# Optimization experiments

Hardware: AMD Instinct MI355X
Metric: run time of the kernel (lower is better)

## Reference

```python
import jax, jax.numpy as jnp
import numpy as np

Q_DIM, K_DIM, H_DIM = 24, 24, 64


def setup_inputs() -> dict:
    key = jax.random.key(0)
    ks = jax.random.split(key, 11)
    B, N, D_OUT = 2048, 512, 128
    s = lambda fan_in: 1.0 / np.sqrt(fan_in)
    inp = {
        "future_weather_patch": jax.random.normal(ks[0], (B, Q_DIM), jnp.float32),
        "past_weather_patches": jax.random.normal(ks[1], (B, N, K_DIM), jnp.float32),
        "transformer_output": jax.random.normal(ks[2], (B, N, D_OUT), jnp.float32),
        # W_Q: Linear(q,h) -> Tanh -> Linear(h,h)
        "wq1": jax.random.uniform(ks[3], (Q_DIM, H_DIM), jnp.float32, -s(Q_DIM), s(Q_DIM)),
        "bq1": jax.random.uniform(ks[4], (H_DIM,), jnp.float32, -s(Q_DIM), s(Q_DIM)),
        "wq2": jax.random.uniform(ks[5], (H_DIM, H_DIM), jnp.float32, -s(H_DIM), s(H_DIM)),
        "bq2": jax.random.uniform(ks[6], (H_DIM,), jnp.float32, -s(H_DIM), s(H_DIM)),
        # W_K: Linear(k,h) -> Tanh -> Linear(h,h)
        "wk1": jax.random.uniform(ks[7], (K_DIM, H_DIM), jnp.float32, -s(K_DIM), s(K_DIM)),
        "bk1": jax.random.uniform(ks[8], (H_DIM,), jnp.float32, -s(K_DIM), s(K_DIM)),
        "wk2": jax.random.uniform(ks[9], (H_DIM, H_DIM), jnp.float32, -s(H_DIM), s(H_DIM)),
        "bk2": jax.random.uniform(ks[10], (H_DIM,), jnp.float32, -s(H_DIM), s(H_DIM)),
    }
    return inp


def reference(future_weather_patch, past_weather_patches, transformer_output,
              wq1, bq1, wq2, bq2, wk1, bk1, wk2, bk2):
    scale = 1.0 / np.sqrt(H_DIM).astype(np.float32)
    # Q: [B, H]  (Linear-Tanh-Linear on the single future patch)
    q = jnp.tanh(future_weather_patch @ wq1 + bq1) @ wq2 + bq2
    # K: [B, N, H]
    k = jnp.tanh(past_weather_patches @ wk1 + bk1) @ wk2 + bk2
    # score: [B, 1, N] = Q . K^T * scale
    score = jnp.einsum("bh,bnh->bn", q, k) * scale
    attn_weights = jax.nn.softmax(score, axis=-1)[:, None, :]  # [B, 1, N]
    # context: [B, D] = attn @ transformer_output
    context = jnp.einsum("bn,bnd->bd", attn_weights[:, 0, :], transformer_output)
    return context, attn_weights
```

## Files before the change

### kernel.cpp

```cpp
#include <hip/hip_runtime.h>
#include <math.h>

#define QD 24
#define KD 24
#define HD 64
#define NN 512
#define DO 128
#define CHUNK 128
#define NCHUNK (NN / CHUNK)

__device__ __forceinline__ float fast_tanh(float x) {
    float ax = __builtin_fabsf(x);
    float t  = __builtin_amdgcn_exp2f(-2.885390081777927f * ax);
    float r  = (1.0f - t) * __builtin_amdgcn_rcpf(1.0f + t);
    return __builtin_copysignf(r, x);
}

__global__ __launch_bounds__(256, 8) void fused_attn(
    const float* __restrict__ fwp,
    const float* __restrict__ pwp,
    const float* __restrict__ to,
    const float* __restrict__ wq1, const float* __restrict__ bq1,
    const float* __restrict__ wq2, const float* __restrict__ bq2,
    const float* __restrict__ wk1, const float* __restrict__ bk1,
    const float* __restrict__ wk2,
    float* __restrict__ out_ctx,
    float* __restrict__ out_attn)
{
    const int b = blockIdx.x;
    const int t = threadIdx.x;

    __shared__ float p_all[NN];
    __shared__ float xf[QD];
    __shared__ float h1[HD];
    __shared__ float qv[HD];
    __shared__ float qks[HD];
    __shared__ float4 part[4][32];

    if (t < QD) xf[t] = fwp[(size_t)b * QD + t];
    __syncthreads();
    if (t < HD) {
        float a = bq1[t];
#pragma unroll
        for (int k = 0; k < QD; ++k) a = fmaf(xf[k], wq1[k * HD + t], a);
        h1[t] = fast_tanh(a);
    }
    __syncthreads();
    if (t < HD) {
        float a = bq2[t];
#pragma unroll
        for (int i = 0; i < HD; ++i) a = fmaf(h1[i], wq2[i * HD + t], a);
        qv[t] = a;
    }
    __syncthreads();
    if (t < HD) {
        float s = 0.0f;
#pragma unroll
        for (int h = 0; h < HD; ++h) s = fmaf(wk2[t * HD + h], qv[h], s);
        qks[t] = s * 0.18033688011112042f;
    }
    __syncthreads();

    float Mb = 0.0f;
#pragma unroll
    for (int h = 0; h < HD; ++h) Mb += __builtin_fabsf(qks[h]);

    const bool is_prod = (t < 128);
    const int ct = t - 128;
    const int g  = ct & 31;
    const int r  = (ct >> 5) & 3;

    const float4* trow = reinterpret_cast<const float4*>(to + (size_t)b * NN * DO) + g;
    float4 acc = make_float4(0.f, 0.f, 0.f, 0.f);

    auto consume = [&](int cc) {
        const int n0 = cc * CHUNK + r * 32;
#pragma unroll 8
        for (int i = 0; i < 32; ++i) {
            const int n = n0 + i;
            const float p = p_all[n];
            float4 v = trow[(size_t)n * (DO / 4)];
            acc.x = fmaf(p, v.x, acc.x);
            acc.y = fmaf(p, v.y, acc.y);
            acc.z = fmaf(p, v.z, acc.z);
            acc.w = fmaf(p, v.w, acc.w);
        }
    };

    const float4* wk1_4 = reinterpret_cast<const float4*>(wk1);
    const float4* bk1_4 = reinterpret_cast<const float4*>(bk1);
    const float4* qks_4 = reinterpret_cast<const float4*>(qks);

    for (int c = 0; c < NCHUNK; ++c) {
        if (is_prod) {
            const int n = c * CHUNK + t;
            const float* prow = pwp + ((size_t)b * NN + n) * KD;
            float x[KD];
#pragma unroll
            for (int i = 0; i < KD / 4; ++i) {
                float4 v = reinterpret_cast<const float4*>(prow)[i];
                x[4 * i + 0] = v.x; x[4 * i + 1] = v.y;
                x[4 * i + 2] = v.z; x[4 * i + 3] = v.w;
            }
            float sc = 0.0f;
#pragma unroll 2
            for (int j4 = 0; j4 < HD / 4; ++j4) {
                float4 bb = bk1_4[j4];
                float a0 = bb.x, a1 = bb.y, a2 = bb.z, a3 = bb.w;
#pragma unroll
                for (int k = 0; k < KD; ++k) {
                    float4 w = wk1_4[k * (HD / 4) + j4];
                    a0 = fmaf(x[k], w.x, a0); a1 = fmaf(x[k], w.y, a1);
                    a2 = fmaf(x[k], w.z, a2); a3 = fmaf(x[k], w.w, a3);
                }
                float4 qq = qks_4[j4];
                sc = fmaf(fast_tanh(a0), qq.x, sc);
                sc = fmaf(fast_tanh(a1), qq.y, sc);
                sc = fmaf(fast_tanh(a2), qq.z, sc);
                sc = fmaf(fast_tanh(a3), qq.w, sc);
            }
            p_all[n] = __builtin_amdgcn_exp2f(sc - Mb);
        } else if (c > 0) {
            consume(c - 1);
        }
        __syncthreads();
    }

    float invL = 0.0f;
    if (!is_prod) {
        consume(NCHUNK - 1);
        part[r][g] = acc;
    } else if (t < 64) {
        float l = 0.0f;
#pragma unroll
        for (int i = 0; i < NN / 64; ++i) l += p_all[t + 64 * i];
#pragma unroll
        for (int o = 32; o > 0; o >>= 1) l += __shfl_xor(l, o, 64);
        invL = __builtin_amdgcn_rcpf(l);
        float* oa = out_attn + (size_t)b * NN;
#pragma unroll
        for (int i = 0; i < NN / 64; ++i) oa[t + 64 * i] = p_all[t + 64 * i] * invL;
    }
    __syncthreads();

    if (t < 32) {
        float4 r0 = part[0][t], r1 = part[1][t], r2 = part[2][t], r3 = part[3][t];
        float4 o;
        o.x = ((r0.x + r1.x) + (r2.x + r3.x)) * invL;
        o.y = ((r0.y + r1.y) + (r2.y + r3.y)) * invL;
        o.z = ((r0.z + r1.z) + (r2.z + r3.z)) * invL;
        o.w = ((r0.w + r1.w) + (r2.w + r3.w)) * invL;
        reinterpret_cast<float4*>(out_ctx + (size_t)b * DO)[t] = o;
    }
}

extern "C" void kernel_launch(void* const* d_in, const int* in_sizes, int n_in,
                              void* d_out, int out_size, void* d_ws, size_t ws_size,
                              hipStream_t stream) {
    const float* fwp = (const float*)d_in[0];
    const float* pwp = (const float*)d_in[1];
    const float* to  = (const float*)d_in[2];
    const float* wq1 = (const float*)d_in[3];
    const float* bq1 = (const float*)d_in[4];
    const float* wq2 = (const float*)d_in[5];
    const float* bq2 = (const float*)d_in[6];
    const float* wk1 = (const float*)d_in[7];
    const float* bk1 = (const float*)d_in[8];
    const float* wk2 = (const float*)d_in[9];

    float* out = (float*)d_out;
    const int B = in_sizes[0] / QD;

    fused_attn<<<B, 256, 0, stream>>>(fwp, pwp, to, wq1, bq1, wq2, bq2,
                                      wk1, bk1, wk2,
                                      out, out + (size_t)B * DO);
}
```

Baseline: 138.6 us.

## Use 512-thread blocks with one key row per thread, drop producer/consumer split

```diff
diff --git a/kernel.cpp b/kernel.cpp
--- a/kernel.cpp
+++ b/kernel.cpp
@@ -6,8 +6,7 @@
 #define HD 64
 #define NN 512
 #define DO 128
-#define CHUNK 128
-#define NCHUNK (NN / CHUNK)
+#define BT 512
 
 __device__ __forceinline__ float fast_tanh(float x) {
     float ax = __builtin_fabsf(x);
@@ -16,7 +15,7 @@
     return __builtin_copysignf(r, x);
 }
 
-__global__ __launch_bounds__(256, 8) void fused_attn(
+__global__ __launch_bounds__(BT, 4) void fused_attn(
     const float* __restrict__ fwp,
     const float* __restrict__ pwp,
     const float* __restrict__ to,
@@ -30,12 +29,21 @@
     const int b = blockIdx.x;
     const int t = threadIdx.x;
 
-    __shared__ float p_all[NN];
     __shared__ float xf[QD];
     __shared__ float h1[HD];
     __shared__ float qv[HD];
     __shared__ float qks[HD];
-    __shared__ float4 part[4][32];
+    __shared__ float p_all[NN];
+    __shared__ float s_red[8];
+    __shared__ float4 part[16][32];
+
+    const float* prow = pwp + ((size_t)b * NN + t) * KD;
+    float4 xv0 = reinterpret_cast<const float4*>(prow)[0];
+    float4 xv1 = reinterpret_cast<const float4*>(prow)[1];
+    float4 xv2 = reinterpret_cast<const float4*>(prow)[2];
+    float4 xv3 = reinterpret_cast<const float4*>(prow)[3];
+    float4 xv4 = reinterpret_cast<const float4*>(prow)[4];
+    float4 xv5 = reinterpret_cast<const float4*>(prow)[5];
 
     if (t < QD) xf[t] = fwp[(size_t)b * QD + t];
     __syncthreads();
@@ -65,91 +73,74 @@
 #pragma unroll
     for (int h = 0; h < HD; ++h) Mb += __builtin_fabsf(qks[h]);
 
-    const bool is_prod = (t < 128);
-    const int ct = t - 128;
-    const int g  = ct & 31;
-    const int r  = (ct >> 5) & 3;
-
-    const float4* trow = reinterpret_cast<const float4*>(to + (size_t)b * NN * DO) + g;
-    float4 acc = make_float4(0.f, 0.f, 0.f, 0.f);
-
-    auto consume = [&](int cc) {
-        const int n0 = cc * CHUNK + r * 32;
-#pragma unroll 8
-        for (int i = 0; i < 32; ++i) {
-            const int n = n0 + i;
-            const float p = p_all[n];
-            float4 v = trow[(size_t)n * (DO / 4)];
-            acc.x = fmaf(p, v.x, acc.x);
-            acc.y = fmaf(p, v.y, acc.y);
-            acc.z = fmaf(p, v.z, acc.z);
-            acc.w = fmaf(p, v.w, acc.w);
-        }
-    };
+    float x[KD];
+    x[0]=xv0.x; x[1]=xv0.y; x[2]=xv0.z; x[3]=xv0.w;
+    x[4]=xv1.x; x[5]=xv1.y; x[6]=xv1.z; x[7]=xv1.w;
+    x[8]=xv2.x; x[9]=xv2.y; x[10]=xv2.z; x[11]=xv2.w;
+    x[12]=xv3.x; x[13]=xv3.y; x[14]=xv3.z; x[15]=xv3.w;
+    x[16]=xv4.x; x[17]=xv4.y; x[18]=xv4.z; x[19]=xv4.w;
+    x[20]=xv5.x; x[21]=xv5.y; x[22]=xv5.z; x[23]=xv5.w;
 
     const float4* wk1_4 = reinterpret_cast<const float4*>(wk1);
     const float4* bk1_4 = reinterpret_cast<const float4*>(bk1);
     const float4* qks_4 = reinterpret_cast<const float4*>(qks);
 
-    for (int c = 0; c < NCHUNK; ++c) {
-        if (is_prod) {
-            const int n = c * CHUNK + t;
-            const float* prow = pwp + ((size_t)b * NN + n) * KD;
-            float x[KD];
+    float sc = 0.0f;
+#pragma unroll 2
+    for (int j4 = 0; j4 < HD / 4; ++j4) {
+        float4 bb = bk1_4[j4];
+        float a0 = bb.x, a1 = bb.y, a2 = bb.z, a3 = bb.w;
 #pragma unroll
-            for (int i = 0; i < KD / 4; ++i) {
-                float4 v = reinterpret_cast<const float4*>(prow)[i];
-                x[4 * i + 0] = v.x; x[4 * i + 1] = v.y;
-                x[4 * i + 2] = v.z; x[4 * i + 3] = v.w;
-            }
-            float sc = 0.0f;
-#pragma unroll 2
-            for (int j4 = 0; j4 < HD / 4; ++j4) {
-                float4 bb = bk1_4[j4];
-                float a0 = bb.x, a1 = bb.y, a2 = bb.z, a3 = bb.w;
+        for (int k = 0; k < KD; ++k) {
+            float4 w = wk1_4[k * (HD / 4) + j4];
+            a0 = fmaf(x[k], w.x, a0); a1 = fmaf(x[k], w.y, a1);
+            a2 = fmaf(x[k], w.z, a2); a3 = fmaf(x[k], w.w, a3);
+        }
+        float4 qq = qks_4[j4];
+        sc = fmaf(fast_tanh(a0), qq.x, sc);
+        sc = fmaf(fast_tanh(a1), qq.y, sc);
+        sc = fmaf(fast_tanh(a2), qq.z, sc);
+        sc = fmaf(fast_tanh(a3), qq.w, sc);
+    }
+    const float p = __builtin_amdgcn_exp2f(sc - Mb);
+    p_all[t] = p;
+
+    float l = p;
 #pragma unroll
-                for (int k = 0; k < KD; ++k) {
-                    float4 w = wk1_4[k * (HD / 4) + j4];
-                    a0 = fmaf(x[k], w.x, a0); a1 = fmaf(x[k], w.y, a1);
-                    a2 = fmaf(x[k], w.z, a2); a3 = fmaf(x[k], w.w, a3);
-                }
-                float4 qq = qks_4[j4];
-                sc = fmaf(fast_tanh(a0), qq.x, sc);
-                sc = fmaf(fast_tanh(a1), qq.y, sc);
-                sc = fmaf(fast_tanh(a2), qq.z, sc);
-                sc = fmaf(fast_tanh(a3), qq.w, sc);
-            }
-            p_all[n] = __builtin_amdgcn_exp2f(sc - Mb);
-        } else if (c > 0) {
-            consume(c - 1);
-        }
-        __syncthreads();
+    for (int o = 32; o > 0; o >>= 1) l += __shfl_xor(l, o, 64);
+    if ((t & 63) == 0) s_red[t >> 6] = l;
+    __syncthreads();
+    const float L = ((s_red[0] + s_red[1]) + (s_red[2] + s_red[3]))
+                  + ((s_red[4] + s_red[5]) + (s_red[6] + s_red[7]));
+    const float invL = __builtin_amdgcn_rcpf(L);
+    out_attn[(size_t)b * NN + t] = p * invL;
+
+    const int g  = t & 31;
+    const int np = t >> 5;
+    const float4* trow = reinterpret_cast<const float4*>(to + (size_t)b * NN * DO) + g;
+    float4 acc = make_float4(0.f, 0.f, 0.f, 0.f);
+#pragma unroll 8
+    for (int i = 0; i < 32; ++i) {
+        const int n = np * 32 + i;
+        const float pp = p_all[n];
+        float4 v = trow[(size_t)n * (DO / 4)];
+        acc.x = fmaf(pp, v.x, acc.x);
+        acc.y = fmaf(pp, v.y, acc.y);
+        acc.z = fmaf(pp, v.z, acc.z);
+        acc.w = fmaf(pp, v.w, acc.w);
     }
-
-    float invL = 0.0f;
-    if (!is_prod) {
-        consume(NCHUNK - 1);
-        part[r][g] = acc;
-    } else if (t < 64) {
-        float l = 0.0f;
-#pragma unroll
-        for (int i = 0; i < NN / 64; ++i) l += p_all[t + 64 * i];
-#pragma unroll
-        for (int o = 32; o > 0; o >>= 1) l += __shfl_xor(l, o, 64);
-        invL = __builtin_amdgcn_rcpf(l);
-        float* oa = out_attn + (size_t)b * NN;
-#pragma unroll
-        for (int i = 0; i < NN / 64; ++i) oa[t + 64 * i] = p_all[t + 64 * i] * invL;
-    }
+    part[np][g] = acc;
     __syncthreads();
 
     if (t < 32) {
-        float4 r0 = part[0][t], r1 = part[1][t], r2 = part[2][t], r3 = part[3][t];
+        float4 r = part[0][t];
+#pragma unroll
+        for (int q = 1; q < 16; ++q) {
+            float4 v = part[q][t];
+            r.x += v.x; r.y += v.y; r.z += v.z; r.w += v.w;
+        }
         float4 o;
-        o.x = ((r0.x + r1.x) + (r2.x + r3.x)) * invL;
-        o.y = ((r0.y + r1.y) + (r2.y + r3.y)) * invL;
-        o.z = ((r0.z + r1.z) + (r2.z + r3.z)) * invL;
-        o.w = ((r0.w + r1.w) + (r2.w + r3.w)) * invL;
+        o.x = r.x * invL; o.y = r.y * invL; o.z = r.z * invL; o.w = r.w * invL;
         reinterpret_cast<float4*>(out_ctx + (size_t)b * DO)[t] = o;
     }
 }
@@ -171,7 +162,7 @@
     float* out = (float*)d_out;
     const int B = in_sizes[0] / QD;
 
-    fused_attn<<<B, 256, 0, stream>>>(fwp, pwp, to, wq1, bq1, wq2, bq2,
-                                      wk1, bk1, wk2,
-                                      out, out + (size_t)B * DO);
+    fused_attn<<<B, BT, 0, stream>>>(fwp, pwp, to, wq1, bq1, wq2, bq2,
+                                     wk1, bk1, wk2,
+                                     out, out + (size_t)B * DO);
 }
```

Result: slower. 153.6 us (+10.8%).

## Split query projection into a separate kernel and lower occupancy hint

Applied to the files above, without the earlier changes.

```diff
diff --git a/kernel.cpp b/kernel.cpp
--- a/kernel.cpp
+++ b/kernel.cpp
@@ -16,54 +16,61 @@
     return __builtin_copysignf(r, x);
 }
 
-__global__ __launch_bounds__(256, 8) void fused_attn(
+__global__ __launch_bounds__(64) void qk_proj(
     const float* __restrict__ fwp,
+    const float* __restrict__ wq1, const float* __restrict__ bq1,
+    const float* __restrict__ wq2, const float* __restrict__ bq2,
+    const float* __restrict__ wk2,
+    float* __restrict__ qks_g, float* __restrict__ Mb_g)
+{
+    const int b = blockIdx.x;
+    const int j = threadIdx.x;
+    __shared__ float xf[QD];
+    __shared__ float h1[HD];
+    __shared__ float qv[HD];
+    if (j < QD) xf[j] = fwp[(size_t)b * QD + j];
+    __syncthreads();
+    float acc = bq1[j];
+#pragma unroll
+    for (int k = 0; k < QD; ++k) acc = fmaf(xf[k], wq1[k * HD + j], acc);
+    h1[j] = fast_tanh(acc);
+    __syncthreads();
+    acc = bq2[j];
+#pragma unroll
+    for (int i = 0; i < HD; ++i) acc = fmaf(h1[i], wq2[i * HD + j], acc);
+    qv[j] = acc;
+    __syncthreads();
+    float s = 0.0f;
+#pragma unroll
+    for (int h = 0; h < HD; ++h) s = fmaf(wk2[j * HD + h], qv[h], s);
+    const float val = s * 0.18033688011112042f;
+    qks_g[(size_t)b * HD + j] = val;
+    float mb = __builtin_fabsf(val);
+#pragma unroll
+    for (int o = 32; o > 0; o >>= 1) mb += __shfl_xor(mb, o, 64);
+    if (j == 0) Mb_g[b] = mb;
+}
+
+__global__ __launch_bounds__(256, 4) void prodcons_attn(
     const float* __restrict__ pwp,
     const float* __restrict__ to,
-    const float* __restrict__ wq1, const float* __restrict__ bq1,
-    const float* __restrict__ wq2, const float* __restrict__ bq2,
-    const float* __restrict__ wk1, const float* __restrict__ bk1,
-    const float* __restrict__ wk2,
+    const float* __restrict__ wk1,
+    const float* __restrict__ bk1,
+    const float* __restrict__ qks_g,
+    const float* __restrict__ Mb_g,
     float* __restrict__ out_ctx,
     float* __restrict__ out_attn)
 {
     const int b = blockIdx.x;
     const int t = threadIdx.x;
 
-    __shared__ float p_all[NN];
-    __shared__ float xf[QD];
-    __shared__ float h1[HD];
-    __shared__ float qv[HD];
-    __shared__ float qks[HD];
+    __shared__ float  p_all[NN];
+    __shared__ float  qks[HD];
     __shared__ float4 part[4][32];
 
-    if (t < QD) xf[t] = fwp[(size_t)b * QD + t];
+    if (t < HD) qks[t] = qks_g[(size_t)b * HD + t];
+    const float Mb = Mb_g[b];
     __syncthreads();
-    if (t < HD) {
-        float a = bq1[t];
-#pragma unroll
-        for (int k = 0; k < QD; ++k) a = fmaf(xf[k], wq1[k * HD + t], a);
-        h1[t] = fast_tanh(a);
-    }
-    __syncthreads();
-    if (t < HD) {
-        float a = bq2[t];
-#pragma unroll
-        for (int i = 0; i < HD; ++i) a = fmaf(h1[i], wq2[i * HD + t], a);
-        qv[t] = a;
-    }
-    __syncthreads();
-    if (t < HD) {
-        float s = 0.0f;
-#pragma unroll
-        for (int h = 0; h < HD; ++h) s = fmaf(wk2[t * HD + h], qv[h], s);
-        qks[t] = s * 0.18033688011112042f;
-    }
-    __syncthreads();
-
-    float Mb = 0.0f;
-#pragma unroll
-    for (int h = 0; h < HD; ++h) Mb += __builtin_fabsf(qks[h]);
 
     const bool is_prod = (t < 128);
     const int ct = t - 128;
@@ -97,11 +104,9 @@
             const float* prow = pwp + ((size_t)b * NN + n) * KD;
             float x[KD];
 #pragma unroll
-            for (int i = 0; i < KD / 4; ++i) {
-                float4 v = reinterpret_cast<const float4*>(prow)[i];
-                x[4 * i + 0] = v.x; x[4 * i + 1] = v.y;
-                x[4 * i + 2] = v.z; x[4 * i + 3] = v.w;
-            }
+            for (int i = 0; i < KD / 4; ++i)
+                reinterpret_cast<float4*>(x)[i] =
+                    reinterpret_cast<const float4*>(prow)[i];
             float sc = 0.0f;
 #pragma unroll 2
             for (int j4 = 0; j4 < HD / 4; ++j4) {
@@ -168,10 +173,15 @@
     const float* bk1 = (const float*)d_in[8];
     const float* wk2 = (const float*)d_in[9];
 
-    float* out = (float*)d_out;
-    const int B = in_sizes[0] / QD;
+    float* out      = (float*)d_out;
+    const int B     = in_sizes[0] / QD;
+    float* out_ctx  = out;
+    float* out_attn = out + (size_t)B * DO;
 
-    fused_attn<<<B, 256, 0, stream>>>(fwp, pwp, to, wq1, bq1, wq2, bq2,
-                                      wk1, bk1, wk2,
-                                      out, out + (size_t)B * DO);
+    float* qks_g = (float*)d_ws;
+    float* Mb_g  = qks_g + (size_t)B * HD;
+
+    qk_proj<<<B, 64, 0, stream>>>(fwp, wq1, bq1, wq2, bq2, wk2, qks_g, Mb_g);
+    prodcons_attn<<<B, 256, 0, stream>>>(pwp, to, wk1, bk1, qks_g, Mb_g,
+                                         out, out + (size_t)B * DO);
 }
```

New measurement: 146.1 us. 5.4% more time.

## Make each wave score its own rows then stream values without block barriers

Applied to the files above, without the earlier changes.

```diff
diff --git a/kernel.cpp b/kernel.cpp
--- a/kernel.cpp
+++ b/kernel.cpp
@@ -6,8 +6,6 @@
 #define HD 64
 #define NN 512
 #define DO 128
-#define CHUNK 128
-#define NCHUNK (NN / CHUNK)
 
 __device__ __forceinline__ float fast_tanh(float x) {
     float ax = __builtin_fabsf(x);
@@ -16,7 +14,7 @@
     return __builtin_copysignf(r, x);
 }
 
-__global__ __launch_bounds__(256, 8) void fused_attn(
+__global__ __launch_bounds__(256, 4) void fused_attn(
     const float* __restrict__ fwp,
     const float* __restrict__ pwp,
     const float* __restrict__ to,
@@ -27,59 +25,96 @@
     float* __restrict__ out_ctx,
     float* __restrict__ out_attn)
 {
-    const int b = blockIdx.x;
-    const int t = threadIdx.x;
+    const int b    = blockIdx.x;
+    const int t    = threadIdx.x;
+    const int wave = t >> 6;
+    const int lane = t & 63;
+    const int g    = lane & 31;
+    const int h    = lane >> 5;
 
-    __shared__ float p_all[NN];
-    __shared__ float xf[QD];
-    __shared__ float h1[HD];
-    __shared__ float qv[HD];
-    __shared__ float qks[HD];
-    __shared__ float4 part[4][32];
+    __shared__ float  qks[HD];
+    __shared__ float  h1s[HD];
+    __shared__ float  qvs[HD];
+    __shared__ float  s_attn[NN];
+    __shared__ float  s_red[4];
+    __shared__ float4 s_part[8][32];
 
-    if (t < QD) xf[t] = fwp[(size_t)b * QD + t];
-    __syncthreads();
+    const int n0 = wave * 64 + lane;
+    const int n1 = n0 + 4 * 64;
+
+    const float* prow0 = pwp + ((size_t)b * NN + n0) * KD;
+    float x[KD];
+#pragma unroll
+    for (int i = 0; i < KD / 4; ++i)
+        reinterpret_cast<float4*>(x)[i] = reinterpret_cast<const float4*>(prow0)[i];
+
     if (t < HD) {
+        float xf[QD];
+#pragma unroll
+        for (int i = 0; i < QD / 4; ++i)
+            reinterpret_cast<float4*>(xf)[i] =
+                reinterpret_cast<const float4*>(fwp + (size_t)b * QD)[i];
         float a = bq1[t];
 #pragma unroll
         for (int k = 0; k < QD; ++k) a = fmaf(xf[k], wq1[k * HD + t], a);
-        h1[t] = fast_tanh(a);
+        h1s[t] = fast_tanh(a);
     }
     __syncthreads();
     if (t < HD) {
         float a = bq2[t];
 #pragma unroll
-        for (int i = 0; i < HD; ++i) a = fmaf(h1[i], wq2[i * HD + t], a);
-        qv[t] = a;
+        for (int i = 0; i < HD; ++i) a = fmaf(h1s[i], wq2[i * HD + t], a);
+        qvs[t] = a;
     }
     __syncthreads();
     if (t < HD) {
         float s = 0.0f;
 #pragma unroll
-        for (int h = 0; h < HD; ++h) s = fmaf(wk2[t * HD + h], qv[h], s);
+        for (int hh = 0; hh < HD; ++hh) s = fmaf(wk2[t * HD + hh], qvs[hh], s);
         qks[t] = s * 0.18033688011112042f;
     }
     __syncthreads();
 
     float Mb = 0.0f;
 #pragma unroll
-    for (int h = 0; h < HD; ++h) Mb += __builtin_fabsf(qks[h]);
+    for (int hh = 0; hh < HD; ++hh) Mb += __builtin_fabsf(qks[hh]);
 
-    const bool is_prod = (t < 128);
-    const int ct = t - 128;
-    const int g  = ct & 31;
-    const int r  = (ct >> 5) & 3;
+    const float4* wk1_4 = reinterpret_cast<const float4*>(wk1);
+    const float4* bk1_4 = reinterpret_cast<const float4*>(bk1);
+    const float4* qks_4 = reinterpret_cast<const float4*>(qks);
+    const float4* trow  = reinterpret_cast<const float4*>(to + (size_t)b * NN * DO) + g;
 
-    const float4* trow = reinterpret_cast<const float4*>(to + (size_t)b * NN * DO) + g;
     float4 acc = make_float4(0.f, 0.f, 0.f, 0.f);
+    float Lloc = 0.0f;
 
-    auto consume = [&](int cc) {
-        const int n0 = cc * CHUNK + r * 32;
+    auto score_one = [&](const float* xr) -> float {
+        float sc = 0.0f;
+#pragma unroll 2
+        for (int j4 = 0; j4 < HD / 4; ++j4) {
+            float4 bb = bk1_4[j4];
+            float a0 = bb.x, a1 = bb.y, a2 = bb.z, a3 = bb.w;
+#pragma unroll
+            for (int k = 0; k < KD; ++k) {
+                float4 w = wk1_4[k * (HD / 4) + j4];
+                a0 = fmaf(xr[k], w.x, a0); a1 = fmaf(xr[k], w.y, a1);
+                a2 = fmaf(xr[k], w.z, a2); a3 = fmaf(xr[k], w.w, a3);
+            }
+            float4 qq = qks_4[j4];
+            sc = fmaf(fast_tanh(a0), qq.x, sc);
+            sc = fmaf(fast_tanh(a1), qq.y, sc);
+            sc = fmaf(fast_tanh(a2), qq.z, sc);
+            sc = fmaf(fast_tanh(a3), qq.w, sc);
+        }
+        return sc;
+    };
+
+    auto stream_chunk = [&](int chunk) {
+        const int base = chunk * 64;
 #pragma unroll 8
         for (int i = 0; i < 32; ++i) {
-            const int n = n0 + i;
-            const float p = p_all[n];
-            float4 v = trow[(size_t)n * (DO / 4)];
+            const int row = base + 2 * i + h;
+            const float p = s_attn[row];
+            float4 v = trow[(size_t)row * (DO / 4)];
             acc.x = fmaf(p, v.x, acc.x);
             acc.y = fmaf(p, v.y, acc.y);
             acc.z = fmaf(p, v.z, acc.z);
@@ -87,69 +122,44 @@
         }
     };
 
-    const float4* wk1_4 = reinterpret_cast<const float4*>(wk1);
-    const float4* bk1_4 = reinterpret_cast<const float4*>(bk1);
-    const float4* qks_4 = reinterpret_cast<const float4*>(qks);
+    const float p0 = __builtin_amdgcn_exp2f(score_one(x) - Mb);
+    s_attn[n0] = p0;
+    Lloc += p0;
 
-    for (int c = 0; c < NCHUNK; ++c) {
-        if (is_prod) {
-            const int n = c * CHUNK + t;
-            const float* prow = pwp + ((size_t)b * NN + n) * KD;
-            float x[KD];
+    const float* prow1 = pwp + ((size_t)b * NN + n1) * KD;
+    float x1[KD];
 #pragma unroll
-            for (int i = 0; i < KD / 4; ++i) {
-                float4 v = reinterpret_cast<const float4*>(prow)[i];
-                x[4 * i + 0] = v.x; x[4 * i + 1] = v.y;
-                x[4 * i + 2] = v.z; x[4 * i + 3] = v.w;
-            }
-            float sc = 0.0f;
-#pragma unroll 2
-            for (int j4 = 0; j4 < HD / 4; ++j4) {
-                float4 bb = bk1_4[j4];
-                float a0 = bb.x, a1 = bb.y, a2 = bb.z, a3 = bb.w;
+    for (int i = 0; i < KD / 4; ++i)
+        reinterpret_cast<float4*>(x1)[i] = reinterpret_cast<const float4*>(prow1)[i];
+
+    stream_chunk(wave);
+
+    const float p1 = __builtin_amdgcn_exp2f(score_one(x1) - Mb);
+    s_attn[n1] = p1;
+    Lloc += p1;
+    stream_chunk(wave + 4);
+
 #pragma unroll
-                for (int k = 0; k < KD; ++k) {
-                    float4 w = wk1_4[k * (HD / 4) + j4];
-                    a0 = fmaf(x[k], w.x, a0); a1 = fmaf(x[k], w.y, a1);
-                    a2 = fmaf(x[k], w.z, a2); a3 = fmaf(x[k], w.w, a3);
-                }
-                float4 qq = qks_4[j4];
-                sc = fmaf(fast_tanh(a0), qq.x, sc);
-                sc = fmaf(fast_tanh(a1), qq.y, sc);
-                sc = fmaf(fast_tanh(a2), qq.z, sc);
-                sc = fmaf(fast_tanh(a3), qq.w, sc);
-            }
-            p_all[n] = __builtin_amdgcn_exp2f(sc - Mb);
-        } else if (c > 0) {
-            consume(c - 1);
-        }
-        __syncthreads();
-    }
-
-    float invL = 0.0f;
-    if (!is_prod) {
-        consume(NCHUNK - 1);
-        part[r][g] = acc;
-    } else if (t < 64) {
-        float l = 0.0f;
-#pragma unroll
-        for (int i = 0; i < NN / 64; ++i) l += p_all[t + 64 * i];
-#pragma unroll
-        for (int o = 32; o > 0; o >>= 1) l += __shfl_xor(l, o, 64);
-        invL = __builtin_amdgcn_rcpf(l);
-        float* oa = out_attn + (size_t)b * NN;
-#pragma unroll
-        for (int i = 0; i < NN / 64; ++i) oa[t + 64 * i] = p_all[t + 64 * i] * invL;
-    }
+    for (int o = 32; o > 0; o >>= 1) Lloc += __shfl_xor(Lloc, o, 64);
+    if (lane == 0) s_red[wave] = Lloc;
+    s_part[wave * 2 + h][g] = acc;
     __syncthreads();
 
+    const float L    = (s_red[0] + s_red[1]) + (s_red[2] + s_red[3]);
+    const float invL = __builtin_amdgcn_rcpf(L);
+
+    out_attn[(size_t)b * NN + t]       = s_attn[t] * invL;
+    out_attn[(size_t)b * NN + t + 256] = s_attn[t + 256] * invL;
+
     if (t < 32) {
-        float4 r0 = part[0][t], r1 = part[1][t], r2 = part[2][t], r3 = part[3][t];
+        float4 r = s_part[0][t];
+#pragma unroll
+        for (int q = 1; q < 8; ++q) {
+            float4 v = s_part[q][t];
+            r.x += v.x; r.y += v.y; r.z += v.z; r.w += v.w;
+        }
         float4 o;
-        o.x = ((r0.x + r1.x) + (r2.x + r3.x)) * invL;
-        o.y = ((r0.y + r1.y) + (r2.y + r3.y)) * invL;
-        o.z = ((r0.z + r1.z) + (r2.z + r3.z)) * invL;
-        o.w = ((r0.w + r1.w) + (r2.w + r3.w)) * invL;
+        o.x = r.x * invL; o.y = r.y * invL; o.z = r.z * invL; o.w = r.w * invL;
         reinterpret_cast<float4*>(out_ctx + (size_t)b * DO)[t] = o;
     }
 }
@@ -168,7 +178,7 @@
     const float* bk1 = (const float*)d_in[8];
     const float* wk2 = (const float*)d_in[9];
 
-    float* out = (float*)d_out;
+    float* out  = (float*)d_out;
     const int B = in_sizes[0] / QD;
 
     fused_attn<<<B, 256, 0, stream>>>(fwp, pwp, to, wq1, bq1, wq2, bq2,
```

New measurement: 132.0 us. -4.8%, faster.
